# Kernel optimization log

Hardware: AMD Instinct MI355X
Metric: run time of the kernel (lower is better)

## Reference

```python
import jax, jax.numpy as jnp
import numpy as np

B, L, D = 8, 2048, 128
K_CURV = 1.0  # Lorentz manifold curvature constant
NEG_INF = float(-2**32 + 1)


def _lorentz_linear(x, W, b, scale):
    # nn.Linear then project onto the Lorentz manifold (dropout is identity in eval).
    x = x @ W.T + b
    time = jax.nn.sigmoid(x[..., :1]) * jnp.exp(scale) + 1.1
    x_narrow = x[..., 1:]
    s = (time * time - K_CURV) / jnp.sum(x_narrow * x_narrow, axis=-1, keepdims=True)
    return jnp.concatenate([time, x_narrow * jnp.sqrt(s)], axis=-1)


def setup_inputs() -> dict:
    key = jax.random.key(0)
    ks = jax.random.split(key, 10)
    stdv = 0.02

    def lin_w(k):
        W = jax.random.uniform(k, (D, D), minval=-stdv, maxval=stdv, dtype=jnp.float32)
        return W.at[:, 0].set(0.0)  # reset_parameters zeros column 0

    inp = {
        'query': jax.random.normal(ks[0], (B, L, D), dtype=jnp.float32),
        'key': jax.random.normal(ks[1], (B, L, D), dtype=jnp.float32),
        'value': jax.random.normal(ks[2], (B, L, D), dtype=jnp.float32),
        'mask': jax.random.bernoulli(ks[3], 0.1, (B, L)),  # True = padded position
        'Wq': lin_w(ks[4]), 'bq': jnp.zeros((D,), jnp.float32), 'sq': jnp.asarray(2.3, jnp.float32),
        'Wk': lin_w(ks[5]), 'bk': jnp.zeros((D,), jnp.float32), 'sk': jnp.asarray(2.3, jnp.float32),
        'Wv': lin_w(ks[6]), 'bv': jnp.zeros((D,), jnp.float32), 'sv': jnp.asarray(2.3, jnp.float32),
        'attn_scale': jnp.asarray([np.sqrt(D)], jnp.float32),
        'attn_bias': jnp.asarray(0.0, jnp.float32),
    }
    return inp


def reference(query, key, value, mask, Wq, bq, sq, Wk, bk, sk, Wv, bv, sv, attn_scale, attn_bias):
    q = _lorentz_linear(query, Wq, bq, sq)  # [B, L, D]
    k = _lorentz_linear(key, Wk, bk, sk)
    v = _lorentz_linear(value, Wv, bv, sv)
    # single head: shape to [B, 1, L, D]
    q, k, v = q[:, None], k[:, None], v[:, None]

    # Lorentzian inner product: negate time component of q
    qk = jnp.einsum('bhqd,bhkd->bhqk', q.at[..., 0].multiply(-1.0), k)
    attn = (2.0 + 2.0 * qk) / attn_scale + attn_bias  # [B, 1, L, L]

    # pad mask [B, L] broadcast over query rows + causal (triu) mask
    pad = jnp.broadcast_to(mask[:, None, :], (B, L, L))
    tri = jnp.triu(jnp.ones((L, L), bool), k=1)
    m = (tri[None] | pad)[:, None]  # [B, 1, L, L]
    attn = jnp.where(m, NEG_INF, attn)
    attn = jax.nn.softmax(attn, axis=-1)

    # Lorentz mid-point: weighted sum, normalize by sqrt(|<ave, ave>_L|)
    ave = jnp.einsum('bhqk,bhkd->bhqd', attn, v)
    lor = -ave[..., :1] ** 2 + jnp.sum(ave[..., 1:] ** 2, axis=-1, keepdims=True)
    denom = jnp.sqrt(jnp.maximum(jnp.abs(-lor), 1e-8))
    out = jnp.sqrt(K_CURV) * ave / denom
    return out[:, 0]  # [B, L, D]
```

## Files before the change

### kernel.cpp

```cpp
#include <hip/hip_runtime.h>

typedef unsigned short u16;
typedef unsigned long long u64;
typedef __attribute__((ext_vector_type(8))) short short8;
typedef __attribute__((ext_vector_type(4))) float f32x4;

#define MFMA16(A,B,C) __builtin_amdgcn_mfma_f32_16x16x32_bf16(A,B,C,0,0,0)
#define NEG_INF_F (-4294967295.0f)

#define Bsz 8
#define Lsz 2048
#define Dsz 128

__device__ __forceinline__ u16 f2bf(float f){
  union { float f; unsigned u; } v; v.f = f;
  unsigned u = v.u;
  return (u16)((u + 0x7fffu + ((u >> 16) & 1u)) >> 16);
}
__device__ __forceinline__ float bf2f(u16 h){
  union { float f; unsigned u; } v; v.u = ((unsigned)h) << 16;
  return v.f;
}

__global__ __launch_bounds__(256) void wconv_kernel(
    const float* __restrict__ Wq, const float* __restrict__ Wk,
    const float* __restrict__ Wv, u16* __restrict__ wb)
{
  int i = blockIdx.x * 256 + threadIdx.x;
  if (i < 16384) wb[i] = f2bf(Wq[i]);
  else if (i < 32768) wb[i] = f2bf(Wk[i - 16384]);
  else if (i < 49152) wb[i] = f2bf(Wv[i - 32768]);
}

#define LPX 136
#define LPY 133

__global__ __launch_bounds__(256) void proj_kernel(
    const float* __restrict__ xq, const float* __restrict__ xk, const float* __restrict__ xv,
    const u16* __restrict__ wb,
    const float* __restrict__ bq, const float* __restrict__ bk, const float* __restrict__ bv,
    const float* __restrict__ sq, const float* __restrict__ sk, const float* __restrict__ sv,
    const float* __restrict__ attn_scale,
    u16* __restrict__ qout, u16* __restrict__ kout,
    u16* __restrict__ vthi, u16* __restrict__ vtlo,
    float* __restrict__ tqo, float* __restrict__ tko,
    float* __restrict__ vpart)
{
  const int z = blockIdx.z;
  const float* x  = (z == 0) ? xq : (z == 1) ? xk : xv;
  const u16*   Wb = wb + z * 16384;
  const float* bb = (z == 0) ? bq : (z == 1) ? bk : bv;
  const float* ss = (z == 0) ? sq : (z == 1) ? sk : sv;

  __shared__ u16  xl[64 * LPX];
  __shared__ u16  wl[128 * LPX];
  __shared__ float yl[64 * LPY];
  __shared__ float scl[64];
  __shared__ float tml[64];

  const int t = threadIdx.x;
  const long row0 = (long)blockIdx.x * 64;

  for (int i = t; i < 2048; i += 256) {
    int r = i >> 4, c8 = (i & 15) * 8;
    *(short8*)&wl[r * LPX + c8] = *(const short8*)&Wb[r * 128 + c8];
  }
  for (int i = t; i < 2048; i += 256) {
    int off = i * 4;
    int r = off >> 7, c = off & 127;
    f32x4 xv4 = *(const f32x4*)(x + row0 * 128 + off);
    u64 wv = (u64)f2bf(xv4[0]) | ((u64)f2bf(xv4[1]) << 16)
           | ((u64)f2bf(xv4[2]) << 32) | ((u64)f2bf(xv4[3]) << 48);
    *(u64*)&xl[r * LPX + c] = wv;
  }
  __syncthreads();

  const int l = t & 63, wid = t >> 6;
  const int qr = l & 15, g = l >> 4;
  const int r0 = wid * 16;

  short8 af[4];
#pragma unroll
  for (int ks = 0; ks < 4; ks++)
    af[ks] = *(const short8*)&xl[(r0 + qr) * LPX + ks * 32 + g * 8];

  f32x4 acc[8];
#pragma unroll
  for (int jt = 0; jt < 8; jt++) acc[jt] = (f32x4){0.f, 0.f, 0.f, 0.f};

#pragma unroll
  for (int ks = 0; ks < 4; ks++) {
#pragma unroll
    for (int jt = 0; jt < 8; jt++) {
      short8 bfr = *(const short8*)&wl[(jt * 16 + qr) * LPX + ks * 32 + g * 8];
      acc[jt] = MFMA16(af[ks], bfr, acc[jt]);
    }
  }

  float bbv[8];
#pragma unroll
  for (int jt = 0; jt < 8; jt++) bbv[jt] = bb[jt * 16 + qr];

  float ssq[4] = {0.f, 0.f, 0.f, 0.f};
#pragma unroll
  for (int jt = 0; jt < 8; jt++)
#pragma unroll
    for (int r = 0; r < 4; r++) {
      float yv = acc[jt][r] + bbv[jt];
      acc[jt][r] = yv;
      float s2 = yv * yv;
      if (jt == 0) s2 = (qr == 0) ? 0.f : s2;
      ssq[r] += s2;
    }
#pragma unroll
  for (int r = 0; r < 4; r++) {
    ssq[r] += __shfl_xor(ssq[r], 1);
    ssq[r] += __shfl_xor(ssq[r], 2);
    ssq[r] += __shfl_xor(ssq[r], 4);
    ssq[r] += __shfl_xor(ssq[r], 8);
  }

  const float es = __expf(ss[0]);
  const float fold = 2.0f / attn_scale[0];

  float tvv[4], sclv[4];
#pragma unroll
  for (int r = 0; r < 4; r++) {
    float y0 = __shfl(acc[0][r], l & 48);
    float tv = es / (1.0f + __expf(-y0)) + 1.1f;
    tvv[r] = tv;
    sclv[r] = sqrtf((tv * tv - 1.0f) / ssq[r]);
  }
  if (qr == 0) {
#pragma unroll
    for (int r = 0; r < 4; r++) {
      tml[r0 + g * 4 + r] = tvv[r];
      scl[r0 + g * 4 + r] = sclv[r];
    }
  }
#pragma unroll
  for (int jt = 0; jt < 8; jt++)
#pragma unroll
    for (int r = 0; r < 4; r++)
      yl[(r0 + g * 4 + r) * LPY + jt * 16 + qr] = acc[jt][r];
  __syncthreads();

  const long gbase = row0 * 128;
  if (z == 0) {
    for (int i = t; i < 64 * 128; i += 256) {
      int r = i >> 7, d = i & 127;
      float v = (d == 0) ? 0.f : yl[r * LPY + d] * scl[r] * fold;
      qout[gbase + i] = f2bf(v);
    }
    if (t < 64) tqo[row0 + t] = -tml[t] * fold;
  } else if (z == 1) {
    for (int i = t; i < 64 * 128; i += 256) {
      int r = i >> 7, d = i & 127;
      float v = (d == 0) ? 0.f : yl[r * LPY + d] * scl[r];
      kout[gbase + i] = f2bf(v);
    }
    if (t < 64) tko[row0 + t] = tml[t];
  } else {
    const int b = (int)(row0 >> 11);
    const int lpos = (int)(row0 & 2047);
    for (int i = t; i < 128 * 64; i += 256) {
      int d = i >> 6, r = i & 63;
      float v = (d == 0) ? tml[r] : yl[r * LPY + d] * scl[r];
      u16 hi = f2bf(v);
      float lo = v - bf2f(hi);
      long idx = ((long)(b * 128 + d)) * 2048 + lpos + r;
      vthi[idx] = hi;
      vtlo[idx] = f2bf(lo);
    }
    if (t < 128) {
      float s = 0.f;
      for (int r = 0; r < 64; r++)
        s += (t == 0) ? tml[r] : yl[r * LPY + t] * scl[r];
      int blk = (int)((row0 >> 6) & 31);
      vpart[((long)(b * 32 + blk)) * 128 + t] = s;
    }
  }
}

__global__ __launch_bounds__(256) void aux_kernel(
    const int* __restrict__ mask, u64* __restrict__ pmask,
    const float* __restrict__ vpart, float* __restrict__ vsum)
{
  int gt = blockIdx.x * 256 + threadIdx.x;
  int wword = gt >> 6;
  int lane = gt & 63;
  if (wword < Bsz * 32) {
    u64 word = __ballot(mask[wword * 64 + lane] != 0);
    if (lane == 0) pmask[wword] = word;
  }
  if (blockIdx.x < 4) {
    int i = blockIdx.x * 256 + threadIdx.x;
    int b = i >> 7, d = i & 127;
    float s = 0.f;
    for (int j = 0; j < 32; j++) s += vpart[((long)(b * 32 + j)) * 128 + d];
    vsum[i] = s;
  }
}

__global__ __launch_bounds__(512, 2) void flash_kernel(
    const u16* __restrict__ qbf, const u16* __restrict__ kb,
    const u16* __restrict__ vthi, const u16* __restrict__ vtlo,
    const float* __restrict__ tq, const float* __restrict__ tk,
    const u64* __restrict__ pmask, const float* __restrict__ vsum,
    const float* __restrict__ sqp, const float* __restrict__ skp,
    const float* __restrict__ asp,
    float* __restrict__ out)
{
  __shared__ u16 Pl[2][32 * 128];
  __shared__ float lLd[8][2][16];
  __shared__ float ssqw[8][2][16];

  const int t = threadIdx.x;
  const int w = t >> 6, l = t & 63;
  const int qr = l & 15, g = l >> 4;
  const int blk = blockIdx.x;
  const int b = blk & 7;
  const int p = (blk >> 3) & 31;
  const int h = blk >> 8;
  const int s = h ? p : (63 - p);
  const int qbase = s * 32;
  const int nkt = (qbase + 159) >> 7;

  const float fold = 2.0f / asp[0];
  const float tqm = __expf(sqp[0]) + 1.1f;
  const float tkm = __expf(skp[0]) + 1.1f;
  const float MS = fold * sqrtf((tqm * tqm - 1.f) * (tkm * tkm - 1.f)) + 1.0f;

  short8 qf[2][4];
  float tqv0, tqv1;
  {
    const u16* qp0 = qbf + ((long)(b * 2048 + qbase + qr)) * 128 + g * 8;
    const u16* qp1 = qp0 + 16 * 128;
#pragma unroll
    for (int ks = 0; ks < 4; ks++) {
      qf[0][ks] = *(const short8*)(qp0 + ks * 32);
      qf[1][ks] = *(const short8*)(qp1 + ks * 32);
    }
    tqv0 = tq[b * 2048 + qbase + qr];
    tqv1 = tq[b * 2048 + qbase + 16 + qr];
  }

  const u16* kbase  = kb   + ((long)(b * 2048 + 16 * w + qr)) * 128 + g * 8;
  const u16* vhbase = vthi + ((long)(b * 128 + 16 * w + qr)) * 2048 + g * 8;
  const u16* vlbase = vtlo + ((long)(b * 128 + 16 * w + qr)) * 2048 + g * 8;

  float lsum0 = 0.f, lsum1 = 0.f;
  f32x4 acc0 = (f32x4){0.f, 0.f, 0.f, 0.f};
  f32x4 acc1 = (f32x4){0.f, 0.f, 0.f, 0.f};

  short8 kc[4], vh[4], vl[4];
#pragma unroll
  for (int ks = 0; ks < 4; ks++) kc[ks] = *(const short8*)(kbase + ks * 32);
  f32x4 tkvc = *(const f32x4*)(tk + b * 2048 + 16 * w + g * 4);
  u64 mwc = pmask[b * 32 + (w >> 2)];

  int cur = 0;
  for (int kt = 0; kt < nkt; kt++) {
    const long k0 = (long)kt << 7;

    f32x4 sv0 = (f32x4){0.f, 0.f, 0.f, 0.f};
    f32x4 sv1 = (f32x4){0.f, 0.f, 0.f, 0.f};
#pragma unroll
    for (int ks = 0; ks < 4; ks++) {
      sv0 = MFMA16(kc[ks], qf[0][ks], sv0);
      sv1 = MFMA16(kc[ks], qf[1][ks], sv1);
    }
    if (kt + 1 < nkt) {
      const u16* kp = kbase + (k0 + 128) * 128;
#pragma unroll
      for (int ks = 0; ks < 4; ks++) kc[ks] = *(const short8*)(kp + ks * 32);
    }

    const bool bndry = (k0 + 127 > qbase);
    float p0[4], p1[4];
#pragma unroll
    for (int r = 0; r < 4; r++) {
      int kl = 16 * w + 4 * g + r;
      bool bad = ((mwc >> (kl & 63)) & 1ull) != 0ull;
      bool bad0 = bad, bad1 = bad;
      if (bndry) {
        bad0 |= (k0 + kl > qbase + qr);
        bad1 |= (k0 + kl > qbase + 16 + qr);
      }
      float e0 = __expf(sv0[r] + tqv0 * tkvc[r] - MS);
      float e1 = __expf(sv1[r] + tqv1 * tkvc[r] - MS);
      p0[r] = bad0 ? 0.f : e0;
      p1[r] = bad1 ? 0.f : e1;
      lsum0 += p0[r];
      lsum1 += p1[r];
    }
    {
      int pch = ((2 * w + (g >> 1)) ^ (qr & 7)) * 8 + (g & 1) * 4;
      u64 w0 = (u64)f2bf(p0[0]) | ((u64)f2bf(p0[1]) << 16)
             | ((u64)f2bf(p0[2]) << 32) | ((u64)f2bf(p0[3]) << 48);
      u64 w1 = (u64)f2bf(p1[0]) | ((u64)f2bf(p1[1]) << 16)
             | ((u64)f2bf(p1[2]) << 32) | ((u64)f2bf(p1[3]) << 48);
      *(u64*)&Pl[cur][qr * 128 + pch] = w0;
      *(u64*)&Pl[cur][(16 + qr) * 128 + pch] = w1;
    }
    if (kt + 1 < nkt) {
      tkvc = *(const f32x4*)(tk + b * 2048 + k0 + 128 + 16 * w + g * 4);
      mwc = pmask[b * 32 + (int)(k0 >> 6) + 2 + (w >> 2)];
    }

    if (kt > 0) {
      const u16* Pb = &Pl[cur ^ 1][0];
#pragma unroll
      for (int ks = 0; ks < 4; ks++) {
        int ch = ((4 * ks + g) ^ (qr & 7)) * 8;
        short8 pf0 = *(const short8*)&Pb[qr * 128 + ch];
        short8 pf1 = *(const short8*)&Pb[(16 + qr) * 128 + ch];
        acc0 = MFMA16(vh[ks], pf0, acc0);
        acc0 = MFMA16(vl[ks], pf0, acc0);
        acc1 = MFMA16(vh[ks], pf1, acc1);
        acc1 = MFMA16(vl[ks], pf1, acc1);
      }
    }

#pragma unroll
    for (int ks = 0; ks < 4; ks++) {
      vh[ks] = *(const short8*)(vhbase + k0 + ks * 32);
      vl[ks] = *(const short8*)(vlbase + k0 + ks * 32);
    }

    asm volatile("s_waitcnt lgkmcnt(0)\n\ts_barrier" ::: "memory");
    cur ^= 1;
  }

  {
    const u16* Pb = &Pl[cur ^ 1][0];
#pragma unroll
    for (int ks = 0; ks < 4; ks++) {
      int ch = ((4 * ks + g) ^ (qr & 7)) * 8;
      short8 pf0 = *(const short8*)&Pb[qr * 128 + ch];
      short8 pf1 = *(const short8*)&Pb[(16 + qr) * 128 + ch];
      acc0 = MFMA16(vh[ks], pf0, acc0);
      acc0 = MFMA16(vl[ks], pf0, acc0);
      acc1 = MFMA16(vh[ks], pf1, acc1);
      acc1 = MFMA16(vl[ks], pf1, acc1);
    }
  }

  lsum0 += __shfl_xor(lsum0, 16); lsum0 += __shfl_xor(lsum0, 32);
  lsum1 += __shfl_xor(lsum1, 16); lsum1 += __shfl_xor(lsum1, 32);
  if (g == 0) { lLd[w][0][qr] = lsum0; lLd[w][1][qr] = lsum1; }
  __syncthreads();

  float Lt0 = 0.f, Lt1 = 0.f;
#pragma unroll
  for (int j = 0; j < 8; j++) { Lt0 += lLd[j][0][qr]; Lt1 += lLd[j][1][qr]; }
  const bool mrow0 = (Lt0 == 0.f);
  const bool mrow1 = (Lt1 == 0.f);
  const float invL0 = mrow0 ? 0.f : 1.0f / Lt0;
  const float invL1 = mrow1 ? 0.f : 1.0f / Lt1;

  const float* vs = vsum + b * 128;
  float av0[4], av1[4];
  float pp0 = 0.f, pp1 = 0.f;
#pragma unroll
  for (int r = 0; r < 4; r++) {
    int d = 16 * w + 4 * g + r;
    float u = vs[d] * (1.0f / 2048.0f);
    float a0 = mrow0 ? u : acc0[r] * invL0;
    float a1 = mrow1 ? u : acc1[r] * invL1;
    av0[r] = a0; av1[r] = a1;
    float sgn = (d == 0) ? -1.f : 1.f;
    pp0 += sgn * a0 * a0;
    pp1 += sgn * a1 * a1;
  }
  pp0 += __shfl_xor(pp0, 16); pp0 += __shfl_xor(pp0, 32);
  pp1 += __shfl_xor(pp1, 16); pp1 += __shfl_xor(pp1, 32);
  if (g == 0) { ssqw[w][0][qr] = pp0; ssqw[w][1][qr] = pp1; }
  __syncthreads();

  float lor0 = 0.f, lor1 = 0.f;
#pragma unroll
  for (int j = 0; j < 8; j++) { lor0 += ssqw[j][0][qr]; lor1 += ssqw[j][1][qr]; }
  float rd0 = 1.0f / sqrtf(fmaxf(fabsf(lor0), 1e-8f));
  float rd1 = 1.0f / sqrtf(fmaxf(fabsf(lor1), 1e-8f));

  float* op0 = out + ((long)(b * 2048 + qbase + qr)) * 128 + 16 * w + 4 * g;
  float* op1 = out + ((long)(b * 2048 + qbase + 16 + qr)) * 128 + 16 * w + 4 * g;
  f32x4 o0, o1;
  o0[0] = av0[0] * rd0; o0[1] = av0[1] * rd0; o0[2] = av0[2] * rd0; o0[3] = av0[3] * rd0;
  o1[0] = av1[0] * rd1; o1[1] = av1[1] * rd1; o1[2] = av1[2] * rd1; o1[3] = av1[3] * rd1;
  *(f32x4*)op0 = o0;
  *(f32x4*)op1 = o1;
}

extern "C" void kernel_launch(void* const* d_in, const int* in_sizes, int n_in,
                              void* d_out, int out_size, void* d_ws, size_t ws_size,
                              hipStream_t stream)
{
  const float* query = (const float*)d_in[0];
  const float* key   = (const float*)d_in[1];
  const float* value = (const float*)d_in[2];
  const int*   mask  = (const int*)d_in[3];
  const float* Wq = (const float*)d_in[4];
  const float* bq = (const float*)d_in[5];
  const float* sq = (const float*)d_in[6];
  const float* Wk = (const float*)d_in[7];
  const float* bk = (const float*)d_in[8];
  const float* sk = (const float*)d_in[9];
  const float* Wv = (const float*)d_in[10];
  const float* bv = (const float*)d_in[11];
  const float* sv = (const float*)d_in[12];
  const float* attn_scale = (const float*)d_in[13];

  float* out = (float*)d_out;
  char* ws = (char*)d_ws;

  float* vsum  = (float*)ws;
  u64*   pmask = (u64*)(ws + 4096);
  float* tqa   = (float*)(ws + 8192);
  float* tka   = (float*)(ws + 8192 + 65536);
  float* vpart = (float*)(ws + 8192 + 131072);
  u16*   wb    = (u16*)(ws + 8192 + 262144);
  char*  big   = ws + 8192 + 262144 + 131072;
  u16*   qbuf  = (u16*)big;
  u16*   kbuf  = qbuf + (size_t)16384 * 128;
  u16*   vthi  = kbuf + (size_t)16384 * 128;
  u16*   vtlo  = vthi + (size_t)16384 * 128;

  wconv_kernel<<<192, 256, 0, stream>>>(Wq, Wk, Wv, wb);
  proj_kernel<<<dim3(256, 1, 3), 256, 0, stream>>>(
      query, key, value, wb, bq, bk, bv, sq, sk, sv, attn_scale,
      qbuf, kbuf, vthi, vtlo, tqa, tka, vpart);
  aux_kernel<<<64, 256, 0, stream>>>(mask, pmask, vpart, vsum);
  flash_kernel<<<512, 512, 0, stream>>>(
      qbuf, kbuf, vthi, vtlo, tqa, tka, pmask, vsum, sq, sk, attn_scale, out);
}
```

Baseline: 113.6 us.

## Feed P from registers into PV MFMA and reduce partial outputs across waves

Removes the shared-memory staging of the probability tile and the per-iteration barrier. Each wave now keeps its own P fragment in registers and uses 16x16x16 bf16 MFMAs against V slices covering all 128 output dims. This needs 8x2 accumulators per wave and a cross-wave shared-memory reduction with 16 barriers at the end. The block-to-query mapping is also simplified to a plain descending order. The trade is higher register pressure, more V global loads per iteration, and an epilogue reduction, in exchange for no LDS P traffic or barrier inside the loop.

```diff
diff --git a/kernel.cpp b/kernel.cpp
--- a/kernel.cpp
+++ b/kernel.cpp
@@ -3,10 +3,15 @@
 typedef unsigned short u16;
 typedef unsigned long long u64;
 typedef __attribute__((ext_vector_type(8))) short short8;
+typedef __attribute__((ext_vector_type(4))) short short4v;
 typedef __attribute__((ext_vector_type(4))) float f32x4;
 
 #define MFMA16(A,B,C) __builtin_amdgcn_mfma_f32_16x16x32_bf16(A,B,C,0,0,0)
-#define NEG_INF_F (-4294967295.0f)
+
+__device__ __forceinline__ f32x4 mfma16k(short4v a, short4v b, f32x4 c){
+  asm("v_mfma_f32_16x16x16_bf16 %0, %1, %2, %0" : "+v"(c) : "v"(a), "v"(b));
+  return c;
+}
 
 #define Bsz 8
 #define Lsz 2048
@@ -211,7 +216,7 @@
     const float* __restrict__ asp,
     float* __restrict__ out)
 {
-  __shared__ u16 Pl[2][32 * 128];
+  __shared__ float mrgL[8][16][34];
   __shared__ float lLd[8][2][16];
   __shared__ float ssqw[8][2][16];
 
@@ -220,9 +225,7 @@
   const int qr = l & 15, g = l >> 4;
   const int blk = blockIdx.x;
   const int b = blk & 7;
-  const int p = (blk >> 3) & 31;
-  const int h = blk >> 8;
-  const int s = h ? p : (63 - p);
+  const int s = 63 - (blk >> 3);
   const int qbase = s * 32;
   const int nkt = (qbase + 159) >> 7;
 
@@ -246,20 +249,23 @@
   }
 
   const u16* kbase  = kb   + ((long)(b * 2048 + 16 * w + qr)) * 128 + g * 8;
-  const u16* vhbase = vthi + ((long)(b * 128 + 16 * w + qr)) * 2048 + g * 8;
-  const u16* vlbase = vtlo + ((long)(b * 128 + 16 * w + qr)) * 2048 + g * 8;
+  const u16* vhbase = vthi + ((long)(b * 128 + qr)) * 2048 + 16 * w + 4 * g;
+  const u16* vlbase = vtlo + ((long)(b * 128 + qr)) * 2048 + 16 * w + 4 * g;
 
   float lsum0 = 0.f, lsum1 = 0.f;
-  f32x4 acc0 = (f32x4){0.f, 0.f, 0.f, 0.f};
-  f32x4 acc1 = (f32x4){0.f, 0.f, 0.f, 0.f};
-
-  short8 kc[4], vh[4], vl[4];
+  f32x4 acc[8][2];
+#pragma unroll
+  for (int f = 0; f < 8; f++) {
+    acc[f][0] = (f32x4){0.f, 0.f, 0.f, 0.f};
+    acc[f][1] = (f32x4){0.f, 0.f, 0.f, 0.f};
+  }
+
+  short8 kc[4];
 #pragma unroll
   for (int ks = 0; ks < 4; ks++) kc[ks] = *(const short8*)(kbase + ks * 32);
   f32x4 tkvc = *(const f32x4*)(tk + b * 2048 + 16 * w + g * 4);
   u64 mwc = pmask[b * 32 + (w >> 2)];
 
-  int cur = 0;
   for (int kt = 0; kt < nkt; kt++) {
     const long k0 = (long)kt << 7;
 
@@ -274,6 +280,13 @@
       const u16* kp = kbase + (k0 + 128) * 128;
 #pragma unroll
       for (int ks = 0; ks < 4; ks++) kc[ks] = *(const short8*)(kp + ks * 32);
+    }
+
+    short4v avh[8], avl[8];
+#pragma unroll
+    for (int f = 0; f < 8; f++) {
+      avh[f] = *(const short4v*)(vhbase + (long)f * 16 * 2048 + k0);
+      avl[f] = *(const short4v*)(vlbase + (long)f * 16 * 2048 + k0);
     }
 
     const bool bndry = (k0 + 127 > qbase);
@@ -294,56 +307,50 @@
       lsum0 += p0[r];
       lsum1 += p1[r];
     }
-    {
-      int pch = ((2 * w + (g >> 1)) ^ (qr & 7)) * 8 + (g & 1) * 4;
-      u64 w0 = (u64)f2bf(p0[0]) | ((u64)f2bf(p0[1]) << 16)
-             | ((u64)f2bf(p0[2]) << 32) | ((u64)f2bf(p0[3]) << 48);
-      u64 w1 = (u64)f2bf(p1[0]) | ((u64)f2bf(p1[1]) << 16)
-             | ((u64)f2bf(p1[2]) << 32) | ((u64)f2bf(p1[3]) << 48);
-      *(u64*)&Pl[cur][qr * 128 + pch] = w0;
-      *(u64*)&Pl[cur][(16 + qr) * 128 + pch] = w1;
-    }
+    short4v pb0, pb1;
+    pb0[0] = (short)f2bf(p0[0]); pb0[1] = (short)f2bf(p0[1]);
+    pb0[2] = (short)f2bf(p0[2]); pb0[3] = (short)f2bf(p0[3]);
+    pb1[0] = (short)f2bf(p1[0]); pb1[1] = (short)f2bf(p1[1]);
+    pb1[2] = (short)f2bf(p1[2]); pb1[3] = (short)f2bf(p1[3]);
+
     if (kt + 1 < nkt) {
       tkvc = *(const f32x4*)(tk + b * 2048 + k0 + 128 + 16 * w + g * 4);
       mwc = pmask[b * 32 + (int)(k0 >> 6) + 2 + (w >> 2)];
     }
 
-    if (kt > 0) {
-      const u16* Pb = &Pl[cur ^ 1][0];
-#pragma unroll
-      for (int ks = 0; ks < 4; ks++) {
-        int ch = ((4 * ks + g) ^ (qr & 7)) * 8;
-        short8 pf0 = *(const short8*)&Pb[qr * 128 + ch];
-        short8 pf1 = *(const short8*)&Pb[(16 + qr) * 128 + ch];
-        acc0 = MFMA16(vh[ks], pf0, acc0);
-        acc0 = MFMA16(vl[ks], pf0, acc0);
-        acc1 = MFMA16(vh[ks], pf1, acc1);
-        acc1 = MFMA16(vl[ks], pf1, acc1);
+#pragma unroll
+    for (int f = 0; f < 8; f++) {
+      acc[f][0] = mfma16k(avh[f], pb0, acc[f][0]);
+      acc[f][0] = mfma16k(avl[f], pb0, acc[f][0]);
+      acc[f][1] = mfma16k(avh[f], pb1, acc[f][1]);
+      acc[f][1] = mfma16k(avl[f], pb1, acc[f][1]);
+    }
+  }
+
+  f32x4 fin0 = (f32x4){0.f, 0.f, 0.f, 0.f};
+  f32x4 fin1 = (f32x4){0.f, 0.f, 0.f, 0.f};
+#pragma unroll
+  for (int f = 0; f < 8; f++) {
+#pragma unroll
+    for (int i = 0; i < 4; i++) {
+      mrgL[w][4 * g + i][qr]      = acc[f][0][i];
+      mrgL[w][4 * g + i][16 + qr] = acc[f][1][i];
+    }
+    __syncthreads();
+    if (w == f) {
+      f32x4 s0 = (f32x4){0.f, 0.f, 0.f, 0.f};
+      f32x4 s1 = (f32x4){0.f, 0.f, 0.f, 0.f};
+#pragma unroll
+      for (int j = 0; j < 8; j++) {
+#pragma unroll
+        for (int i = 0; i < 4; i++) {
+          s0[i] += mrgL[j][4 * g + i][qr];
+          s1[i] += mrgL[j][4 * g + i][16 + qr];
+        }
       }
-    }
-
-#pragma unroll
-    for (int ks = 0; ks < 4; ks++) {
-      vh[ks] = *(const short8*)(vhbase + k0 + ks * 32);
-      vl[ks] = *(const short8*)(vlbase + k0 + ks * 32);
-    }
-
-    asm volatile("s_waitcnt lgkmcnt(0)\n\ts_barrier" ::: "memory");
-    cur ^= 1;
-  }
-
-  {
-    const u16* Pb = &Pl[cur ^ 1][0];
-#pragma unroll
-    for (int ks = 0; ks < 4; ks++) {
-      int ch = ((4 * ks + g) ^ (qr & 7)) * 8;
-      short8 pf0 = *(const short8*)&Pb[qr * 128 + ch];
-      short8 pf1 = *(const short8*)&Pb[(16 + qr) * 128 + ch];
-      acc0 = MFMA16(vh[ks], pf0, acc0);
-      acc0 = MFMA16(vl[ks], pf0, acc0);
-      acc1 = MFMA16(vh[ks], pf1, acc1);
-      acc1 = MFMA16(vl[ks], pf1, acc1);
-    }
+      fin0 = s0; fin1 = s1;
+    }
+    __syncthreads();
   }
 
   lsum0 += __shfl_xor(lsum0, 16); lsum0 += __shfl_xor(lsum0, 32);
@@ -366,8 +373,8 @@
   for (int r = 0; r < 4; r++) {
     int d = 16 * w + 4 * g + r;
     float u = vs[d] * (1.0f / 2048.0f);
-    float a0 = mrow0 ? u : acc0[r] * invL0;
-    float a1 = mrow1 ? u : acc1[r] * invL1;
+    float a0 = mrow0 ? u : fin0[r] * invL0;
+    float a1 = mrow1 ? u : fin1[r] * invL1;
     av0[r] = a0; av1[r] = a1;
     float sgn = (d == 0) ? -1.f : 1.f;
     pp0 += sgn * a0 * a0;
```

New measurement: 139.7 us. +23.0%, slower.
